# Optimization experiments

Measured on AMD Instinct MI355X. Metric: run time of the kernel, lower is better.

The kernel has to match this reference:

```python
import jax, jax.numpy as jnp
import numpy as np

NEG_SLOPE = 0.2

def _gat_layer(x, src, dst, W, a_src, a_dst, b, heads, out_ch, num_nodes):
    # x: [N, F_in] -> h: [N, H, C]
    h = (x @ W).reshape(num_nodes, heads, out_ch)
    alpha_s = jnp.sum(h * a_src, axis=-1)  # [N, H]
    alpha_d = jnp.sum(h * a_dst, axis=-1)  # [N, H]
    e = jax.nn.leaky_relu(alpha_s[src] + alpha_d[dst], NEG_SLOPE)  # [E, H]
    # segment softmax over edges grouped by destination node
    seg_max = jax.ops.segment_max(e, dst, num_segments=num_nodes)
    seg_max = jnp.where(jnp.isfinite(seg_max), seg_max, 0.0)
    e = jnp.exp(e - jax.lax.stop_gradient(seg_max)[dst])
    denom = jax.ops.segment_sum(e, dst, num_segments=num_nodes)
    alpha = e / (denom[dst] + 1e-16)  # [E, H]
    msgs = h[src] * alpha[:, :, None]  # [E, H, C]
    out = jax.ops.segment_sum(msgs, dst, num_segments=num_nodes)  # [N, H, C]
    return out.reshape(num_nodes, heads * out_ch) + b


def setup_inputs() -> dict:
    key = jax.random.key(0)
    ks = jax.random.split(key, 11)
    N, E, F, H, C = 100000, 1600000, 128, 4, 32
    x = jax.random.normal(ks[0], (N, F), dtype=jnp.float32)
    edge_index = jax.random.randint(ks[1], (2, E), 0, N, dtype=jnp.int64)
    s = 0.1
    return {
        "x": x,
        "edge_index": edge_index,
        "W1": jax.random.normal(ks[2], (F, H * C), dtype=jnp.float32) * s,
        "att_src1": jax.random.normal(ks[3], (H, C), dtype=jnp.float32) * s,
        "att_dst1": jax.random.normal(ks[4], (H, C), dtype=jnp.float32) * s,
        "b1": jax.random.normal(ks[5], (H * C,), dtype=jnp.float32) * s,
        "W2": jax.random.normal(ks[6], (H * C, F), dtype=jnp.float32) * s,
        "att_src2": jax.random.normal(ks[7], (1, F), dtype=jnp.float32) * s,
        "att_dst2": jax.random.normal(ks[8], (1, F), dtype=jnp.float32) * s,
        "b2": jax.random.normal(ks[9], (F,), dtype=jnp.float32) * s,
    }


def reference(x, edge_index, W1, att_src1, att_dst1, b1, W2, att_src2, att_dst2, b2):
    N = x.shape[0]
    H, C = att_src1.shape
    F = x.shape[1]
    # PyG GATConv adds self-loops by default
    loop = jnp.arange(N, dtype=edge_index.dtype)
    src = jnp.concatenate([edge_index[0], loop])
    dst = jnp.concatenate([edge_index[1], loop])
    # dropout is identity in eval mode (training=False)
    h = _gat_layer(x, src, dst, W1, att_src1, att_dst1, b1, H, C, N)
    out = _gat_layer(h, src, dst, W2, att_src2, att_dst2, b2, 1, F, N)
    return out
```

## Files before the change

### kernel.cpp

```cpp
#include <hip/hip_runtime.h>
#include <cstdint>
#include <cstddef>

#define NEG_SLOPE 0.2f

typedef __attribute__((ext_vector_type(8))) short short8;
typedef __attribute__((ext_vector_type(4))) float f32x4;

__device__ __forceinline__ float lrelu(float v) { return v > 0.0f ? v : NEG_SLOPE * v; }

__device__ __forceinline__ unsigned short f2bf(float f) {
  unsigned u = __float_as_uint(f);
  unsigned r = (u + 0x7fff + ((u >> 16) & 1)) >> 16;
  return (unsigned short)r;
}
__device__ __forceinline__ float bf2f(unsigned short u) {
  return __uint_as_float((unsigned)u << 16);
}
__device__ __forceinline__ unsigned pack2bf(float a, float b) {
  return (unsigned)f2bf(a) | ((unsigned)f2bf(b) << 16);
}

__device__ __forceinline__ float selh4(float4 v, int h) {
  return (h == 0) ? v.x : (h == 1) ? v.y : (h == 2) ? v.z : v.w;
}

__global__ __launch_bounds__(256) void prep(const float* __restrict__ W1,
                                            const float* __restrict__ W2,
                                            unsigned short* __restrict__ WT1,
                                            unsigned short* __restrict__ WT2,
                                            int* __restrict__ cnt, int N) {
  int i = blockIdx.x * 256 + threadIdx.x;
  if (i < 16384) {
    int n = i >> 7, k = i & 127;
    WT1[i] = f2bf(W1[k * 128 + n]);
  } else if (i < 32768) {
    int j = i - 16384;
    int n = j >> 7, k = j & 127;
    WT2[j] = f2bf(W2[k * 128 + n]);
  }
  if (i < N) cnt[i] = 0;
}

template <int H, bool BF16IN>
__global__ __launch_bounds__(256) void gemm_mfma(const void* __restrict__ Xv,
                                                 const unsigned short* __restrict__ WT,
                                                 unsigned short* __restrict__ Ybf,
                                                 const float* __restrict__ Asrc,
                                                 const float* __restrict__ Adst,
                                                 float* __restrict__ AS,
                                                 float* __restrict__ AD, int N) {
  __shared__ unsigned short xs[64 * 136];
  __shared__ unsigned short wsh[128 * 136];
  __shared__ float ash[128];
  __shared__ float adh[128];
  const int tid = threadIdx.x;
  const int rowBase = blockIdx.x * 64;
  const int rowsHere = min(64, N - rowBase);

  if (tid < 128) ash[tid] = Asrc[tid];
  else adh[tid - 128] = Adst[tid - 128];

#pragma unroll
  for (int it = 0; it < 8; ++it) {
    int idx = it * 256 + tid;
    int n = idx >> 4, k16 = idx & 15;
    *(uint4*)(wsh + n * 136 + k16 * 8) = *(const uint4*)(WT + (size_t)n * 128 + k16 * 8);
  }
  if constexpr (BF16IN) {
    const unsigned short* Xb = (const unsigned short*)Xv;
#pragma unroll
    for (int it = 0; it < 4; ++it) {
      int idx = it * 256 + tid;
      int r = idx >> 4, c8 = idx & 15;
      uint4 v = make_uint4(0, 0, 0, 0);
      if (r < rowsHere) v = *(const uint4*)(Xb + (size_t)(rowBase + r) * 128 + c8 * 8);
      *(uint4*)(xs + r * 136 + c8 * 8) = v;
    }
  } else {
    const float* Xf = (const float*)Xv;
#pragma unroll
    for (int it = 0; it < 8; ++it) {
      int idx = it * 256 + tid;
      int r = idx >> 5, c4 = idx & 31;
      float4 v = make_float4(0.f, 0.f, 0.f, 0.f);
      if (r < rowsHere) v = *(const float4*)(Xf + (size_t)(rowBase + r) * 128 + c4 * 4);
      ushort4 bv;
      bv.x = f2bf(v.x); bv.y = f2bf(v.y); bv.z = f2bf(v.z); bv.w = f2bf(v.w);
      *(ushort4*)(xs + r * 136 + c4 * 4) = bv;
    }
  }
  __syncthreads();

  const int lane = tid & 63;
  const int w = tid >> 6;
  const int m15 = lane & 15;
  const int quad = lane >> 4;
  f32x4 acc[8];
#pragma unroll
  for (int t = 0; t < 8; ++t) acc[t] = (f32x4){0.f, 0.f, 0.f, 0.f};

#pragma unroll
  for (int k0 = 0; k0 < 128; k0 += 32) {
    short8 a = *(const short8*)(xs + (16 * w + m15) * 136 + k0 + quad * 8);
#pragma unroll
    for (int t = 0; t < 8; ++t) {
      short8 b = *(const short8*)(wsh + (t * 16 + m15) * 136 + k0 + quad * 8);
      acc[t] = __builtin_amdgcn_mfma_f32_16x16x32_bf16(a, b, acc[t], 0, 0, 0);
    }
  }

  __syncthreads();
#pragma unroll
  for (int t = 0; t < 8; ++t) {
#pragma unroll
    for (int r = 0; r < 4; ++r) {
      int row = 16 * w + quad * 4 + r;
      xs[row * 136 + t * 16 + m15] = f2bf(acc[t][r]);
    }
  }
  __syncthreads();
#pragma unroll
  for (int it = 0; it < 4; ++it) {
    int idx = it * 256 + tid;
    int r = idx >> 4, c8 = idx & 15;
    if (r < rowsHere)
      *(uint4*)(Ybf + (size_t)(rowBase + r) * 128 + c8 * 8) = *(const uint4*)(xs + r * 136 + c8 * 8);
  }

  {
    const int r = tid >> 2;
    const int part = tid & 3;
    if (r < rowsHere) {
      const unsigned short* hp = xs + r * 136 + part * 32;
      float as = 0.f, ad = 0.f;
#pragma unroll
      for (int c4 = 0; c4 < 4; ++c4) {
        uint4 hw = *(const uint4*)(hp + c4 * 8);
        unsigned wds[4] = {hw.x, hw.y, hw.z, hw.w};
#pragma unroll
        for (int k = 0; k < 4; ++k) {
          const int c = part * 32 + c4 * 8 + k * 2;
          float v0 = bf2f((unsigned short)wds[k]);
          float v1 = bf2f((unsigned short)(wds[k] >> 16));
          as += v0 * ash[c] + v1 * ash[c + 1];
          ad += v0 * adh[c] + v1 * adh[c + 1];
        }
      }
      if (H == 4) {
        AS[(size_t)(rowBase + r) * 4 + part] = as;
        AD[(size_t)(rowBase + r) * 4 + part] = ad;
      } else {
        as += __shfl_xor(as, 1, 4);
        as += __shfl_xor(as, 2, 4);
        ad += __shfl_xor(ad, 1, 4);
        ad += __shfl_xor(ad, 2, 4);
        if (part == 0) { AS[rowBase + r] = as; AD[rowBase + r] = ad; }
      }
    }
  }
}

__global__ __launch_bounds__(256) void csr_count(const int* __restrict__ ei, int E, int Etot,
                                                 int* __restrict__ cnt) {
  int e = blockIdx.x * 256 + threadIdx.x;
  if (e >= Etot) return;
  int d = (e < E) ? ei[E + e] : (e - E);
  atomicAdd(&cnt[d], 1);
}

__global__ __launch_bounds__(256) void scan_blocks(const int* __restrict__ cnt,
                                                   int* __restrict__ rowStart,
                                                   int* __restrict__ blockSums, int N) {
  __shared__ int sh[256];
  const int tid = threadIdx.x;
  const int i = blockIdx.x * 256 + tid;
  int v = (i < N) ? cnt[i] : 0;
  sh[tid] = v;
  __syncthreads();
  for (int o = 1; o < 256; o <<= 1) {
    int t = (tid >= o) ? sh[tid - o] : 0;
    __syncthreads();
    sh[tid] += t;
    __syncthreads();
  }
  if (i < N) rowStart[i] = sh[tid] - v;
  if (tid == 255) blockSums[blockIdx.x] = sh[255];
}

__global__ __launch_bounds__(256) void scan_sums(int* __restrict__ bs, int nb) {
  __shared__ int sh[256];
  __shared__ int carryS;
  const int tid = threadIdx.x;
  if (tid == 0) carryS = 0;
  __syncthreads();
  for (int c = 0; c < nb; c += 256) {
    int i = c + tid;
    int v = (i < nb) ? bs[i] : 0;
    sh[tid] = v;
    __syncthreads();
    for (int o = 1; o < 256; o <<= 1) {
      int t = (tid >= o) ? sh[tid - o] : 0;
      __syncthreads();
      sh[tid] += t;
      __syncthreads();
    }
    int carry = carryS;
    if (i < nb) bs[i] = carry + sh[tid] - v;
    int total = sh[255];
    __syncthreads();
    if (tid == 0) carryS = carry + total;
    __syncthreads();
  }
}

__global__ __launch_bounds__(256) void add_offsets(int* __restrict__ rowStart,
                                                   const int* __restrict__ bs,
                                                   int* __restrict__ cursor, int N, int Etot) {
  int i = blockIdx.x * 256 + threadIdx.x;
  if (i == 0) rowStart[N] = Etot;
  if (i >= N) return;
  int r = rowStart[i] + bs[i >> 8];
  rowStart[i] = r;
  cursor[i] = r;
}

#define SCAT_CHUNK 2048
__global__ __launch_bounds__(256) void csr_scatter_x(const int* __restrict__ ei, int E, int Etot,
                                                     int* __restrict__ cursor,
                                                     int* __restrict__ srcS, int nper) {
  const int xcd = blockIdx.x & 7;
  const int lo = xcd * nper;
  const int hi = lo + nper;
  const int e0 = (blockIdx.x >> 3) * SCAT_CHUNK + threadIdx.x;
#pragma unroll
  for (int it = 0; it < SCAT_CHUNK / 256; ++it) {
    int e = e0 + it * 256;
    if (e < Etot) {
      int d = (e < E) ? ei[E + e] : (e - E);
      if (d >= lo && d < hi) {
        int s = (e < E) ? ei[e] : d;
        int pos = atomicAdd(&cursor[d], 1);
        srcS[pos] = s;
      }
    }
  }
}

template <int H, bool OUTBF>
__global__ __launch_bounds__(256) void gat_node(
    const int* __restrict__ rowStart, const int* __restrict__ srcS,
    const float* __restrict__ AS, const float* __restrict__ AD,
    const unsigned short* __restrict__ Hbf, const float* __restrict__ B,
    void* __restrict__ Out, int N) {
  const int g = threadIdx.x >> 4;
  const int n = blockIdx.x * 16 + g;
  if (n >= N) return;
  const int l = threadIdx.x & 15;
  const int beg = rowStart[n];
  const int end = rowStart[n + 1];
  const int f0 = l * 8;
  const int myh = (H == 4) ? (l >> 2) : 0;

  float4 adv = make_float4(0.f, 0.f, 0.f, 0.f);
  if (H == 4) adv = *(const float4*)(AD + (size_t)n * 4);
  else adv.x = AD[n];

  float4 m = make_float4(-INFINITY, -INFINITY, -INFINITY, -INFINITY);
  for (int i = beg + l; i < end; i += 16) {
    const int s = srcS[i];
    if (H == 4) {
      float4 as = *(const float4*)(AS + (size_t)s * 4);
      m.x = fmaxf(m.x, lrelu(as.x + adv.x));
      m.y = fmaxf(m.y, lrelu(as.y + adv.y));
      m.z = fmaxf(m.z, lrelu(as.z + adv.z));
      m.w = fmaxf(m.w, lrelu(as.w + adv.w));
    } else {
      m.x = fmaxf(m.x, lrelu(AS[s] + adv.x));
    }
  }
#pragma unroll
  for (int o = 8; o >= 1; o >>= 1) {
    m.x = fmaxf(m.x, __shfl_xor(m.x, o, 16));
    if (H == 4) {
      m.y = fmaxf(m.y, __shfl_xor(m.y, o, 16));
      m.z = fmaxf(m.z, __shfl_xor(m.z, o, 16));
      m.w = fmaxf(m.w, __shfl_xor(m.w, o, 16));
    }
  }
  const float m_my  = (H == 4) ? selh4(m, myh)   : m.x;
  const float ad_my = (H == 4) ? selh4(adv, myh) : adv.x;

  float den = 0.f;
  float acc[8];
#pragma unroll
  for (int k = 0; k < 8; ++k) acc[k] = 0.f;

  auto ISSUE = [&](int ib, int (&sj)[8], float (&pv)[8], uint4 (&hv)[8]) {
#pragma unroll
    for (int q = 0; q < 8; ++q) {
      int idx = ib + q;
      sj[q] = srcS[idx < end ? idx : beg];
    }
#pragma unroll
    for (int q = 0; q < 8; ++q)
      hv[q] = *(const uint4*)(Hbf + (size_t)sj[q] * 128 + f0);
#pragma unroll
    for (int q = 0; q < 8; ++q) {
      const float a = (H == 4) ? AS[(size_t)sj[q] * 4 + myh] : AS[sj[q]];
      float p = __expf(lrelu(a + ad_my) - m_my);
      pv[q] = (ib + q < end) ? p : 0.f;
    }
  };
  auto CONSUME = [&](float (&pv)[8], uint4 (&hv)[8]) {
#pragma unroll
    for (int q = 0; q < 8; ++q) {
      const float aj = pv[q];
      den += aj;
      acc[0] += bf2f((unsigned short)hv[q].x) * aj;
      acc[1] += bf2f((unsigned short)(hv[q].x >> 16)) * aj;
      acc[2] += bf2f((unsigned short)hv[q].y) * aj;
      acc[3] += bf2f((unsigned short)(hv[q].y >> 16)) * aj;
      acc[4] += bf2f((unsigned short)hv[q].z) * aj;
      acc[5] += bf2f((unsigned short)(hv[q].z >> 16)) * aj;
      acc[6] += bf2f((unsigned short)hv[q].w) * aj;
      acc[7] += bf2f((unsigned short)(hv[q].w >> 16)) * aj;
    }
  };

  int sjA[8], sjB[8];
  float pvA[8], pvB[8];
  uint4 hvA[8], hvB[8];
  int i = beg;
  ISSUE(i, sjA, pvA, hvA);
  for (;;) {
    int inext = i + 8;
    if (inext < end) ISSUE(inext, sjB, pvB, hvB);
    CONSUME(pvA, hvA);
    i = inext;
    if (i >= end) break;
    inext = i + 8;
    if (inext < end) ISSUE(inext, sjA, pvA, hvA);
    CONSUME(pvB, hvB);
    i = inext;
    if (i >= end) break;
  }

  const float inv = 1.0f / (den + 1e-16f);
  float o[8];
#pragma unroll
  for (int k = 0; k < 8; ++k) o[k] = acc[k] * inv + B[f0 + k];
  if constexpr (OUTBF) {
    uint4 wv;
    wv.x = pack2bf(o[0], o[1]);
    wv.y = pack2bf(o[2], o[3]);
    wv.z = pack2bf(o[4], o[5]);
    wv.w = pack2bf(o[6], o[7]);
    *(uint4*)((unsigned short*)Out + (size_t)n * 128 + f0) = wv;
  } else {
    float* Of = (float*)Out;
    float4 o0, o1;
    o0.x = o[0]; o0.y = o[1]; o0.z = o[2]; o0.w = o[3];
    o1.x = o[4]; o1.y = o[5]; o1.z = o[6]; o1.w = o[7];
    *(float4*)(Of + (size_t)n * 128 + f0) = o0;
    *(float4*)(Of + (size_t)n * 128 + f0 + 4) = o1;
  }
}

extern "C" void kernel_launch(void* const* d_in, const int* in_sizes, int n_in,
                              void* d_out, int out_size, void* d_ws, size_t ws_size,
                              hipStream_t stream) {
  const float* x    = (const float*)d_in[0];
  const int*   ei   = (const int*)d_in[1];
  const float* W1   = (const float*)d_in[2];
  const float* as1w = (const float*)d_in[3];
  const float* ad1w = (const float*)d_in[4];
  const float* b1   = (const float*)d_in[5];
  const float* W2   = (const float*)d_in[6];
  const float* as2w = (const float*)d_in[7];
  const float* ad2w = (const float*)d_in[8];
  const float* b2   = (const float*)d_in[9];

  const int N = in_sizes[0] / 128;
  const int E = in_sizes[1] / 2;
  const int Etot = E + N;
  const int nb = (N + 255) / 256;

  char* ws = (char*)d_ws;
  size_t off = 0;
  auto alloc = [&](size_t bytes) -> void* {
    void* p = ws + off;
    off = (off + bytes + 255) & ~(size_t)255;
    return p;
  };
  unsigned short* Hbf   = (unsigned short*)alloc((size_t)N * 128 * 2);
  unsigned short* out1b = (unsigned short*)alloc((size_t)N * 128 * 2);
  float* AS1  = (float*)alloc((size_t)N * 4 * 4);
  float* AD1  = (float*)alloc((size_t)N * 4 * 4);
  float* AS2  = (float*)alloc((size_t)N * 4);
  float* AD2  = (float*)alloc((size_t)N * 4);
  unsigned short* WT1 = (unsigned short*)alloc(128 * 128 * 2);
  unsigned short* WT2 = (unsigned short*)alloc(128 * 128 * 2);
  int*   cnt      = (int*)alloc((size_t)N * 4);
  int*   rowStart = (int*)alloc((size_t)(N + 1) * 4);
  int*   cursor   = (int*)alloc((size_t)N * 4);
  int*   blockSums= (int*)alloc((size_t)nb * 4);
  int*   srcS     = (int*)alloc((size_t)Etot * 4);

  const int prepBlocks = (max(32768, N) + 255) / 256;
  prep<<<prepBlocks, 256, 0, stream>>>(W1, W2, WT1, WT2, cnt, N);

  const int ebBlocks = (Etot + 255) / 256;
  csr_count<<<ebBlocks, 256, 0, stream>>>(ei, E, Etot, cnt);
  scan_blocks<<<nb, 256, 0, stream>>>(cnt, rowStart, blockSums, N);
  scan_sums<<<1, 256, 0, stream>>>(blockSums, nb);
  add_offsets<<<nb, 256, 0, stream>>>(rowStart, blockSums, cursor, N, Etot);
  const int nper = (N + 7) / 8;
  const int scatBlocks = 8 * ((Etot + SCAT_CHUNK - 1) / SCAT_CHUNK);
  csr_scatter_x<<<scatBlocks, 256, 0, stream>>>(ei, E, Etot, cursor, srcS, nper);

  const int gemmBlocks = (N + 63) / 64;
  const int nodeBlocks = (N + 15) / 16;

  gemm_mfma<4, false><<<gemmBlocks, 256, 0, stream>>>(x, WT1, Hbf, as1w, ad1w, AS1, AD1, N);
  gat_node<4, true><<<nodeBlocks, 256, 0, stream>>>(rowStart, srcS, AS1, AD1, Hbf, b1, out1b, N);

  gemm_mfma<1, true><<<gemmBlocks, 256, 0, stream>>>(out1b, WT2, Hbf, as2w, ad2w, AS2, AD2, N);
  gat_node<1, false><<<nodeBlocks, 256, 0, stream>>>(rowStart, srcS, AS2, AD2, Hbf, b2, d_out, N);
}
```

Before: 447.1 us.

## Drop segment-max pass and map one wavefront per node in GAT aggregation

The aggregation kernel no longer computes the per-destination max before the softmax. It exponentiates the leaky-ReLU scores directly, which removes a full extra gather pass over each node's edges. The thread mapping also changes from 16 lanes per node handling 8 features each to a 64-lane wavefront per node handling 2 features each, with an occupancy hint. Dropping the max subtraction risks overflow in exp when scores are large, and each lane now issues more, smaller loads.

After: 571.6 us. +27.9%, slower.

```diff
diff --git a/kernel.cpp b/kernel.cpp
--- a/kernel.cpp
+++ b/kernel.cpp
@@ -19,10 +19,6 @@
 }
 __device__ __forceinline__ unsigned pack2bf(float a, float b) {
   return (unsigned)f2bf(a) | ((unsigned)f2bf(b) << 16);
-}
-
-__device__ __forceinline__ float selh4(float4 v, int h) {
-  return (h == 0) ? v.x : (h == 1) ? v.y : (h == 2) ? v.z : v.w;
 }
 
 __global__ __launch_bounds__(256) void prep(const float* __restrict__ W1,
@@ -248,122 +244,67 @@
 }
 
 template <int H, bool OUTBF>
-__global__ __launch_bounds__(256) void gat_node(
+__global__ __launch_bounds__(256, 8) void gat_node(
     const int* __restrict__ rowStart, const int* __restrict__ srcS,
     const float* __restrict__ AS, const float* __restrict__ AD,
     const unsigned short* __restrict__ Hbf, const float* __restrict__ B,
     void* __restrict__ Out, int N) {
-  const int g = threadIdx.x >> 4;
-  const int n = blockIdx.x * 16 + g;
+  const int wid = threadIdx.x >> 6;
+  const int n = blockIdx.x * 4 + wid;
   if (n >= N) return;
-  const int l = threadIdx.x & 15;
+  const int lane = threadIdx.x & 63;
+  const int c0 = lane * 2;
+  const int myh = (H == 4) ? (lane >> 4) : 0;
   const int beg = rowStart[n];
   const int end = rowStart[n + 1];
-  const int f0 = l * 8;
-  const int myh = (H == 4) ? (l >> 2) : 0;
-
-  float4 adv = make_float4(0.f, 0.f, 0.f, 0.f);
-  if (H == 4) adv = *(const float4*)(AD + (size_t)n * 4);
-  else adv.x = AD[n];
-
-  float4 m = make_float4(-INFINITY, -INFINITY, -INFINITY, -INFINITY);
-  for (int i = beg + l; i < end; i += 16) {
-    const int s = srcS[i];
-    if (H == 4) {
-      float4 as = *(const float4*)(AS + (size_t)s * 4);
-      m.x = fmaxf(m.x, lrelu(as.x + adv.x));
-      m.y = fmaxf(m.y, lrelu(as.y + adv.y));
-      m.z = fmaxf(m.z, lrelu(as.z + adv.z));
-      m.w = fmaxf(m.w, lrelu(as.w + adv.w));
-    } else {
-      m.x = fmaxf(m.x, lrelu(AS[s] + adv.x));
-    }
-  }
-#pragma unroll
-  for (int o = 8; o >= 1; o >>= 1) {
-    m.x = fmaxf(m.x, __shfl_xor(m.x, o, 16));
-    if (H == 4) {
-      m.y = fmaxf(m.y, __shfl_xor(m.y, o, 16));
-      m.z = fmaxf(m.z, __shfl_xor(m.z, o, 16));
-      m.w = fmaxf(m.w, __shfl_xor(m.w, o, 16));
-    }
-  }
-  const float m_my  = (H == 4) ? selh4(m, myh)   : m.x;
-  const float ad_my = (H == 4) ? selh4(adv, myh) : adv.x;
-
-  float den = 0.f;
-  float acc[8];
-#pragma unroll
-  for (int k = 0; k < 8; ++k) acc[k] = 0.f;
-
-  auto ISSUE = [&](int ib, int (&sj)[8], float (&pv)[8], uint4 (&hv)[8]) {
+  const float ad_my = (H == 4) ? AD[(size_t)n * 4 + myh] : AD[n];
+
+  float den = 0.f, acc0 = 0.f, acc1 = 0.f;
+
+  auto ISSUE = [&](int ib, unsigned (&hw)[8], float (&av)[8]) {
 #pragma unroll
     for (int q = 0; q < 8; ++q) {
       int idx = ib + q;
-      sj[q] = srcS[idx < end ? idx : beg];
-    }
-#pragma unroll
-    for (int q = 0; q < 8; ++q)
-      hv[q] = *(const uint4*)(Hbf + (size_t)sj[q] * 128 + f0);
+      const int s = srcS[idx < end ? idx : beg];
+      hw[q] = *(const unsigned*)(Hbf + (size_t)s * 128 + c0);
+      av[q] = (H == 4) ? AS[(size_t)s * 4 + myh] : AS[s];
+    }
+  };
+  auto CONSUME = [&](int ib, unsigned (&hw)[8], float (&av)[8]) {
 #pragma unroll
     for (int q = 0; q < 8; ++q) {
-      const float a = (H == 4) ? AS[(size_t)sj[q] * 4 + myh] : AS[sj[q]];
-      float p = __expf(lrelu(a + ad_my) - m_my);
-      pv[q] = (ib + q < end) ? p : 0.f;
+      float p = (ib + q < end) ? __expf(lrelu(av[q] + ad_my)) : 0.f;
+      den += p;
+      acc0 += bf2f((unsigned short)hw[q]) * p;
+      acc1 += bf2f((unsigned short)(hw[q] >> 16)) * p;
     }
   };
-  auto CONSUME = [&](float (&pv)[8], uint4 (&hv)[8]) {
-#pragma unroll
-    for (int q = 0; q < 8; ++q) {
-      const float aj = pv[q];
-      den += aj;
-      acc[0] += bf2f((unsigned short)hv[q].x) * aj;
-      acc[1] += bf2f((unsigned short)(hv[q].x >> 16)) * aj;
-      acc[2] += bf2f((unsigned short)hv[q].y) * aj;
-      acc[3] += bf2f((unsigned short)(hv[q].y >> 16)) * aj;
-      acc[4] += bf2f((unsigned short)hv[q].z) * aj;
-      acc[5] += bf2f((unsigned short)(hv[q].z >> 16)) * aj;
-      acc[6] += bf2f((unsigned short)hv[q].w) * aj;
-      acc[7] += bf2f((unsigned short)(hv[q].w >> 16)) * aj;
-    }
-  };
-
-  int sjA[8], sjB[8];
-  float pvA[8], pvB[8];
-  uint4 hvA[8], hvB[8];
+
+  unsigned hwA[8], hwB[8];
+  float avA[8], avB[8];
   int i = beg;
-  ISSUE(i, sjA, pvA, hvA);
+  ISSUE(i, hwA, avA);
   for (;;) {
     int inext = i + 8;
-    if (inext < end) ISSUE(inext, sjB, pvB, hvB);
-    CONSUME(pvA, hvA);
+    if (inext < end) ISSUE(inext, hwB, avB);
+    CONSUME(i, hwA, avA);
     i = inext;
     if (i >= end) break;
     inext = i + 8;
-    if (inext < end) ISSUE(inext, sjA, pvA, hvA);
-    CONSUME(pvB, hvB);
+    if (inext < end) ISSUE(inext, hwA, avA);
+    CONSUME(i, hwB, avB);
     i = inext;
     if (i >= end) break;
   }
 
   const float inv = 1.0f / (den + 1e-16f);
-  float o[8];
-#pragma unroll
-  for (int k = 0; k < 8; ++k) o[k] = acc[k] * inv + B[f0 + k];
+  const float2 bv = *(const float2*)(B + c0);
+  const float o0 = acc0 * inv + bv.x;
+  const float o1 = acc1 * inv + bv.y;
   if constexpr (OUTBF) {
-    uint4 wv;
-    wv.x = pack2bf(o[0], o[1]);
-    wv.y = pack2bf(o[2], o[3]);
-    wv.z = pack2bf(o[4], o[5]);
-    wv.w = pack2bf(o[6], o[7]);
-    *(uint4*)((unsigned short*)Out + (size_t)n * 128 + f0) = wv;
+    *((unsigned*)Out + (size_t)n * 64 + lane) = pack2bf(o0, o1);
   } else {
-    float* Of = (float*)Out;
-    float4 o0, o1;
-    o0.x = o[0]; o0.y = o[1]; o0.z = o[2]; o0.w = o[3];
-    o1.x = o[4]; o1.y = o[5]; o1.z = o[6]; o1.w = o[7];
-    *(float4*)(Of + (size_t)n * 128 + f0) = o0;
-    *(float4*)(Of + (size_t)n * 128 + f0 + 4) = o1;
+    *(float2*)((float*)Out + (size_t)n * 128 + c0) = make_float2(o0, o1);
   }
 }
 
@@ -420,7 +361,7 @@
   csr_scatter_x<<<scatBlocks, 256, 0, stream>>>(ei, E, Etot, cursor, srcS, nper);
 
   const int gemmBlocks = (N + 63) / 64;
-  const int nodeBlocks = (N + 15) / 16;
+  const int nodeBlocks = (N + 3) / 4;
 
   gemm_mfma<4, false><<<gemmBlocks, 256, 0, stream>>>(x, WT1, Hbf, as1w, ad1w, AS1, AD1, N);
   gat_node<4, true><<<nodeBlocks, 256, 0, stream>>>(rowStart, srcS, AS1, AD1, Hbf, b1, out1b, N);
```
